# Kernel tuning notes

Hardware: AMD Instinct MI355X
Metric: run time of the kernel (lower is better)

The kernel has to match this reference:

```python
import jax, jax.numpy as jnp
import numpy as np

Nw, Nt, IN_DIM, OUT_DIM, H, FEAT = 200000, 20000, 128, 256, 8, 64
DH = OUT_DIM // H
DEG = 32
E = Nt * DEG
FFN = 512
NEG_SLOPE = 0.01  # F.leaky_relu default


def setup_inputs() -> dict:
    key = jax.random.key(0)
    ks = jax.random.split(key, 12)
    w = jax.random.normal(ks[0], (Nw, IN_DIM), jnp.float32)
    t = jax.random.normal(ks[1], (Nt, OUT_DIM), jnp.float32)
    topic_feat = jax.random.normal(ks[2], (Nt, FEAT), jnp.float32)
    edge_src = jax.random.randint(ks[3], (E,), 0, Nw)
    # every topic node gets exactly DEG in-edges (sorted dst, no empty segments)
    edge_dst = jnp.repeat(jnp.arange(Nt), DEG)
    s = lambda k, sh, f: jax.random.normal(k, sh, jnp.float32) * np.float32(f)
    fc_w = s(ks[4], (H, IN_DIM, DH), 1.0 / np.sqrt(IN_DIM))
    attn_a = s(ks[5], (H, 2 * DH), 1.0 / np.sqrt(2 * DH))
    dstfeat_w = s(ks[6], (H, FEAT, DH), 1.0 / np.sqrt(FEAT))
    proj_w = s(ks[7], (2 * OUT_DIM, OUT_DIM), 1.0 / np.sqrt(2 * OUT_DIM))
    proj_b = jnp.zeros((OUT_DIM,), jnp.float32)
    ffn_w1 = s(ks[8], (OUT_DIM, FFN), 1.0 / np.sqrt(OUT_DIM))
    ffn_b1 = jnp.zeros((FFN,), jnp.float32)
    ffn_w2 = s(ks[9], (FFN, OUT_DIM), 1.0 / np.sqrt(FFN))
    ffn_b2 = jnp.zeros((OUT_DIM,), jnp.float32)
    ln_scale = jnp.ones((OUT_DIM,), jnp.float32)
    ln_bias = jnp.zeros((OUT_DIM,), jnp.float32)
    return dict(w=w, t=t, topic_feat=topic_feat, edge_src=edge_src, edge_dst=edge_dst,
                fc_w=fc_w, attn_a=attn_a, dstfeat_w=dstfeat_w, proj_w=proj_w, proj_b=proj_b,
                ffn_w1=ffn_w1, ffn_b1=ffn_b1, ffn_w2=ffn_w2, ffn_b2=ffn_b2,
                ln_scale=ln_scale, ln_bias=ln_bias)


def reference(w, t, topic_feat, edge_src, edge_dst, fc_w, attn_a, dstfeat_w,
              proj_w, proj_b, ffn_w1, ffn_b1, ffn_w2, ffn_b2, ln_scale, ln_bias):
    # per-head projections: z on word (src) nodes, dstfeat on topic (dst) nodes
    z = jnp.einsum('ni,hid->hnd', w, fc_w)              # [H, Nw, DH]
    dz = jnp.einsum('nf,hfd->hnd', topic_feat, dstfeat_w)  # [H, Nt, DH]
    # attn_fc(cat(z_src, dstfeat)) decomposes into per-node dot products
    s_src = jnp.einsum('hnd,hd->hn', z, attn_a[:, :DH])   # [H, Nw]
    s_dst = jnp.einsum('hnd,hd->hn', dz, attn_a[:, DH:])  # [H, Nt]
    e = s_src[:, edge_src] + s_dst[:, edge_dst]           # [H, E]
    e = jnp.where(e >= 0, e, NEG_SLOPE * e)               # leaky_relu
    # segment softmax over incoming edges of each dst node (DGL mailbox softmax)
    seg_max = jax.vmap(lambda v: jax.ops.segment_max(v, edge_dst, num_segments=Nt))(e)
    seg_max = jnp.where(jnp.isfinite(seg_max), seg_max, 0.0)  # guard empty segments
    p = jnp.exp(e - seg_max[:, edge_dst])
    denom = jax.vmap(lambda v: jax.ops.segment_sum(v, edge_dst, num_segments=Nt))(p)
    alpha = p / jnp.maximum(denom[:, edge_dst], 1e-9)     # [H, E]
    msg = alpha[:, :, None] * z[:, edge_src, :]           # [H, E, DH]
    agg = jax.vmap(lambda m: jax.ops.segment_sum(m, edge_dst, num_segments=Nt))(msg)  # [H, Nt, DH]
    h = jnp.transpose(agg, (1, 0, 2)).reshape(Nt, OUT_DIM)  # head concat
    h = jax.nn.elu(h)
    h = jnp.concatenate([h, t], axis=-1) @ proj_w + proj_b  # [Nt, OUT_DIM]
    # PositionwiseFeedForward: LN -> gelu -> linear -> residual (dropout off in eval)
    mu = jnp.mean(h, axis=-1, keepdims=True)
    var = jnp.var(h, axis=-1, keepdims=True)
    xn = (h - mu) / jnp.sqrt(var + 1e-6) * ln_scale + ln_bias
    inter = jax.nn.gelu(xn @ ffn_w1 + ffn_b1, approximate=False)
    return (inter @ ffn_w2 + ffn_b2) + h
```

## Files before the change

### kernel.cpp

```cpp
#include <hip/hip_runtime.h>
#include <hip/hip_bf16.h>

typedef __attribute__((ext_vector_type(8))) short short8v;
typedef __attribute__((ext_vector_type(4))) float f32x4;

#define NW 200000
#define NT 20000
#define KIN 128
#define ODIM 256
#define NH 8
#define DH_ 32
#define FEAT_ 64
#define DEG_ 32
#define FFN_ 512

#define WS_Z     0ull
#define WS_SSRC  102400000ull
#define WS_SDST  108800000ull
#define WS_HBF   109440000ull
#define WS_TBF   119680000ull
#define WS_B1T   129920000ull
#define WS_PWT   129985536ull
#define WS_W1T   130247680ull
#define WS_W2T   130509824ull
#define WS_ABT   130771968ull

__device__ __forceinline__ unsigned short f2bf(float x) {
    __hip_bfloat16 b = __float2bfloat16(x);
    return *reinterpret_cast<unsigned short*>(&b);
}
__device__ __forceinline__ float bf2f(unsigned short u) {
    unsigned int v = ((unsigned int)u) << 16;
    return __uint_as_float(v);
}

__global__ __launch_bounds__(256) void prep_w(const float* __restrict__ fc_w,
        const float* __restrict__ proj_w, const float* __restrict__ w1,
        const float* __restrict__ w2, const float* __restrict__ attn_a,
        unsigned short* __restrict__ b1f, unsigned short* __restrict__ pwf,
        unsigned short* __restrict__ w1f, unsigned short* __restrict__ w2f,
        unsigned short* __restrict__ abt) {
    int i = blockIdx.x * 256 + threadIdx.x;
    int j = i & 7, l = (i >> 3) & 63;
    int l16 = l & 15, lq = l >> 4;
    if (i < 32768) {
        int kk = (i >> 9) & 3, g = i >> 11;
        int c = g * 16 + l16, k = kk * 32 + lq * 8 + j;
        int h = c >> 5, d = c & 31;
        b1f[i] = f2bf(fc_w[(h * KIN + k) * DH_ + d]);
    }
    if (i < 4096) {
        int h = i >> 8, k = i & 255;
        abt[i] = ((k >> 5) == h) ? f2bf(attn_a[h * 64 + (k & 31)]) : (unsigned short)0;
    }
    {
        int kk = (i >> 9) & 15, g = i >> 13;
        int c = g * 16 + l16, k = kk * 32 + lq * 8 + j;
        pwf[i] = f2bf(proj_w[(size_t)k * ODIM + c]);
    }
    {
        int kk = (i >> 9) & 7, g = i >> 12;
        int c = g * 16 + l16, k = kk * 32 + lq * 8 + j;
        w1f[i] = f2bf(w1[(size_t)k * FFN_ + c]);
    }
    {
        int kk = (i >> 9) & 15, g = i >> 13;
        int c = g * 16 + l16, k = kk * 32 + lq * 8 + j;
        w2f[i] = f2bf(w2[(size_t)k * ODIM + c]);
    }
}

__global__ __launch_bounds__(256) void prep_t(const float* __restrict__ t,
                                              unsigned short* __restrict__ tbf) {
    int i = blockIdx.x * 256 + threadIdx.x;
    const float4* p = (const float4*)(t + (size_t)i * 8);
    float4 a = p[0], b = p[1];
    short8v o;
    o[0] = (short)f2bf(a.x); o[1] = (short)f2bf(a.y);
    o[2] = (short)f2bf(a.z); o[3] = (short)f2bf(a.w);
    o[4] = (short)f2bf(b.x); o[5] = (short)f2bf(b.y);
    o[6] = (short)f2bf(b.z); o[7] = (short)f2bf(b.w);
    *((short8v*)tbf + i) = o;
}

#define ZRP 264
#define TPB 5
__global__ __launch_bounds__(256) void k1_z(const float* __restrict__ w,
        const unsigned short* __restrict__ b1f, const unsigned short* __restrict__ abt,
        unsigned short* __restrict__ z, float* __restrict__ s_src) {
    __shared__ unsigned short aS[2][64 * 136];
    __shared__ unsigned short zR[64 * ZRP];
    const int tid = threadIdx.x;
    const int wv = tid >> 6, l = tid & 63;
    const int l16 = l & 15, lq = l >> 4;
    const int tile0 = blockIdx.x * TPB;
    float4 vb[8];
    #pragma unroll
    for (int j = 0; j < 8; ++j) {
        int i = tid + j * 256;
        int r = i >> 5, kq = i & 31;
        vb[j] = *(const float4*)(w + (size_t)(tile0 * 64 + r) * KIN + kq * 4);
    }
    #pragma unroll
    for (int j = 0; j < 8; ++j) {
        int i = tid + j * 256;
        int r = i >> 5, kq = i & 31;
        ushort4 u;
        u.x = f2bf(vb[j].x); u.y = f2bf(vb[j].y);
        u.z = f2bf(vb[j].z); u.w = f2bf(vb[j].w);
        *(ushort4*)(&aS[0][r * 136 + kq * 4]) = u;
    }
    for (int t = 0; t < TPB; ++t) {
        const int cur = t & 1;
        const int row0 = (tile0 + t) * 64;
        if (t < TPB - 1) {
            #pragma unroll
            for (int j = 0; j < 8; ++j) {
                int i = tid + j * 256;
                int r = i >> 5, kq = i & 31;
                vb[j] = *(const float4*)(w + (size_t)(row0 + 64 + r) * KIN + kq * 4);
            }
        }
        __syncthreads();
        f32x4 acc[4][4];
        #pragma unroll
        for (int a = 0; a < 4; ++a)
            #pragma unroll
            for (int b = 0; b < 4; ++b)
                acc[a][b] = (f32x4){0.f, 0.f, 0.f, 0.f};
        #pragma unroll
        for (int kk = 0; kk < 4; ++kk) {
            short8v af[4], bfr[4];
            #pragma unroll
            for (int rf = 0; rf < 4; ++rf)
                af[rf] = *(const short8v*)(&aS[cur][(rf * 16 + l16) * 136 + kk * 32 + lq * 8]);
            #pragma unroll
            for (int cf = 0; cf < 4; ++cf)
                bfr[cf] = *(const short8v*)((const short*)b1f +
                            ((((wv * 4 + cf) * 4 + kk) << 9) + l * 8));
            #pragma unroll
            for (int rf = 0; rf < 4; ++rf)
                #pragma unroll
                for (int cf = 0; cf < 4; ++cf)
                    acc[rf][cf] = __builtin_amdgcn_mfma_f32_16x16x32_bf16(
                        af[rf], bfr[cf], acc[rf][cf], 0, 0, 0);
        }
        #pragma unroll
        for (int rl = 0; rl < 4; ++rl)
            #pragma unroll
            for (int cf = 0; cf < 4; ++cf) {
                int c = wv * 64 + cf * 16 + l16;
                #pragma unroll
                for (int q = 0; q < 4; ++q) {
                    int row = rl * 16 + lq * 4 + q;
                    int pc = c ^ ((row & 8) << 1);
                    zR[row * ZRP + pc] = f2bf(acc[rl][cf][q]);
                }
            }
        __syncthreads();
        {
            const int base = wv * 16;
            const int rsw = (l16 & 8) << 1;
            f32x4 sacc = (f32x4){0.f, 0.f, 0.f, 0.f};
            #pragma unroll
            for (int kk = 0; kk < 8; ++kk) {
                int kc = (kk * 32 + lq * 8) ^ rsw;
                short8v a = *(const short8v*)(&zR[(base + l16) * ZRP + kc]);
                short8v b = *(const short8v*)((const short*)abt + (size_t)l16 * 256 + kk * 32 + lq * 8);
                sacc = __builtin_amdgcn_mfma_f32_16x16x32_bf16(a, b, sacc, 0, 0, 0);
            }
            if (l16 < NH) {
                #pragma unroll
                for (int q = 0; q < 4; ++q)
                    s_src[(size_t)(row0 + base + lq * 4 + q) * NH + l16] = sacc[q];
            }
        }
        #pragma unroll
        for (int j = 0; j < 8; ++j) {
            int idx = tid + j * 256;
            int r = idx >> 5, ch = idx & 31;
            int pc = (ch * 8) ^ ((r & 8) << 1);
            short8v v = *(const short8v*)(&zR[r * ZRP + pc]);
            *(short8v*)(z + (size_t)(row0 + r) * ODIM + ch * 8) = v;
        }
        if (t < TPB - 1) {
            #pragma unroll
            for (int j = 0; j < 8; ++j) {
                int i = tid + j * 256;
                int r = i >> 5, kq = i & 31;
                ushort4 u;
                u.x = f2bf(vb[j].x); u.y = f2bf(vb[j].y);
                u.z = f2bf(vb[j].z); u.w = f2bf(vb[j].w);
                *(ushort4*)(&aS[cur ^ 1][r * 136 + kq * 4]) = u;
            }
        }
    }
}

__global__ __launch_bounds__(256) void k_sdst(const float* __restrict__ topic_feat,
        const float* __restrict__ dstfeat_w, const float* __restrict__ attn_a,
        float* __restrict__ s_dst) {
    __shared__ float rS[NH * 65];
    __shared__ float tfS[32 * 65];
    const int tid = threadIdx.x;
    for (int i = tid; i < NH * FEAT_; i += 256) {
        int h = i >> 6, f = i & 63;
        const float* dw = dstfeat_w + (size_t)(h * FEAT_ + f) * DH_;
        const float* aa = attn_a + h * 64 + DH_;
        float s = 0.f;
        #pragma unroll
        for (int d = 0; d < DH_; ++d) s += dw[d] * aa[d];
        rS[h * 65 + f] = s;
    }
    const int n0 = blockIdx.x * 32;
    for (int i = tid; i < 32 * FEAT_; i += 256) {
        int n = i >> 6, f = i & 63;
        tfS[n * 65 + f] = topic_feat[(size_t)(n0 + n) * FEAT_ + f];
    }
    __syncthreads();
    int n = tid >> 3, h = tid & 7;
    float s = 0.f;
    #pragma unroll
    for (int f = 0; f < FEAT_; ++f) s += tfS[n * 65 + f] * rS[h * 65 + f];
    s_dst[(size_t)(n0 + n) * NH + h] = s;
}

__global__ __launch_bounds__(256) void k2_attn(const int* __restrict__ edge_src,
        const float* __restrict__ s_src, const float* __restrict__ s_dst,
        const unsigned short* __restrict__ z, unsigned short* __restrict__ hbf) {
    __shared__ int srcS[4][32];
    __shared__ float aS[4][32][8];
    const int tid = threadIdx.x;
    const int nd = tid >> 6, l = tid & 63;
    const int n = blockIdx.x * 4 + nd;
    if (l < 32) srcS[nd][l] = edge_src[(size_t)n * DEG_ + l];
    __syncthreads();
    {
        int e = l & 31, h0 = (l >> 5) * 4;
        int s = srcS[nd][e];
        float4 ss = *(const float4*)(s_src + (size_t)s * NH + h0);
        float4 sd = *(const float4*)(s_dst + (size_t)n * NH + h0);
        float v[4] = {ss.x + sd.x, ss.y + sd.y, ss.z + sd.z, ss.w + sd.w};
        #pragma unroll
        for (int j = 0; j < 4; ++j) v[j] = (v[j] >= 0.f) ? v[j] : 0.01f * v[j];
        float al[4];
        #pragma unroll
        for (int j = 0; j < 4; ++j) {
            float m = v[j];
            #pragma unroll
            for (int off = 16; off >= 1; off >>= 1)
                m = fmaxf(m, __shfl_xor(m, off));
            float p = expf(v[j] - m);
            float su = p;
            #pragma unroll
            for (int off = 16; off >= 1; off >>= 1)
                su += __shfl_xor(su, off);
            al[j] = p / fmaxf(su, 1e-9f);
        }
        float4 a4 = {al[0], al[1], al[2], al[3]};
        *(float4*)(&aS[nd][e][h0]) = a4;
    }
    __syncthreads();
    {
        const int half = l >> 5, cl = l & 31;
        const int head = cl >> 2;
        float acc[8];
        #pragma unroll
        for (int j = 0; j < 8; ++j) acc[j] = 0.f;
        #pragma unroll 4
        for (int ee = 0; ee < 16; ++ee) {
            int e = ee * 2 + half;
            float a = aS[nd][e][head];
            int sp = srcS[nd][e];
            short8v zv = *(const short8v*)(z + (size_t)sp * ODIM + cl * 8);
            #pragma unroll
            for (int j = 0; j < 8; ++j)
                acc[j] += a * bf2f((unsigned short)zv[j]);
        }
        #pragma unroll
        for (int j = 0; j < 8; ++j)
            acc[j] += __shfl_xor(acc[j], 32);
        if (half == 0) {
            short8v o;
            #pragma unroll
            for (int j = 0; j < 8; ++j) {
                float v = (acc[j] > 0.f) ? acc[j] : expm1f(acc[j]);
                o[j] = (short)f2bf(v);
            }
            *(short8v*)(hbf + (size_t)n * ODIM + cl * 8) = o;
        }
    }
}

#define BUFP 524
#define XNP  268
__global__ __launch_bounds__(256, 3) void k34_ffn(const unsigned short* __restrict__ hbf,
        const unsigned short* __restrict__ tbf, const unsigned short* __restrict__ pwf,
        const float* __restrict__ proj_b, const float* __restrict__ ln_scale,
        const float* __restrict__ ln_bias, const unsigned short* __restrict__ w1f,
        const float* __restrict__ b1, const unsigned short* __restrict__ w2f,
        const float* __restrict__ b2, float* __restrict__ out) {
    __shared__ unsigned short buf[32 * BUFP];
    __shared__ unsigned short xnS[32 * XNP];
    __shared__ float lnP[4][32], lnQ[4][32];
    __shared__ float muS[32], rsS[32];
    const int tid = threadIdx.x;
    const int row0 = blockIdx.x * 32;
    #pragma unroll
    for (int j = 0; j < 8; ++j) {
        int i = tid + j * 256;
        int r = i >> 6, cq = i & 63;
        ushort4 hv = *(const ushort4*)(hbf + (size_t)(row0 + r) * ODIM + cq * 4);
        *(ushort4*)(&buf[r * BUFP + cq * 4]) = hv;
        ushort4 tv = *(const ushort4*)(tbf + (size_t)(row0 + r) * ODIM + cq * 4);
        *(ushort4*)(&buf[r * BUFP + 256 + cq * 4]) = tv;
    }
    __syncthreads();
    const int wv = tid >> 6, l = tid & 63;
    const int l16 = l & 15, lq = l >> 4;
    const int l8 = l * 8;
    f32x4 acc0[2][4];
    #pragma unroll
    for (int rf = 0; rf < 2; ++rf)
        #pragma unroll
        for (int cf = 0; cf < 4; ++cf) acc0[rf][cf] = (f32x4){0.f, 0.f, 0.f, 0.f};
    {
        short8v bp[2][4];
        #pragma unroll
        for (int cf = 0; cf < 4; ++cf)
            bp[0][cf] = *(const short8v*)((const short*)pwf + ((((wv * 4 + cf) * 16) << 9) + l8));
        #pragma unroll
        for (int kk = 0; kk < 16; ++kk) {
            const int cur = kk & 1;
            if (kk < 15) {
                #pragma unroll
                for (int cf = 0; cf < 4; ++cf)
                    bp[cur ^ 1][cf] = *(const short8v*)((const short*)pwf +
                        ((((wv * 4 + cf) * 16 + kk + 1) << 9) + l8));
            }
            short8v a0 = *(const short8v*)(&buf[l16 * BUFP + kk * 32 + lq * 8]);
            short8v a1 = *(const short8v*)(&buf[(16 + l16) * BUFP + kk * 32 + lq * 8]);
            #pragma unroll
            for (int cf = 0; cf < 4; ++cf) {
                acc0[0][cf] = __builtin_amdgcn_mfma_f32_16x16x32_bf16(a0, bp[cur][cf], acc0[0][cf], 0, 0, 0);
                acc0[1][cf] = __builtin_amdgcn_mfma_f32_16x16x32_bf16(a1, bp[cur][cf], acc0[1][cf], 0, 0, 0);
            }
        }
    }
    #pragma unroll
    for (int cf = 0; cf < 4; ++cf) {
        float bb = proj_b[wv * 64 + cf * 16 + l16];
        #pragma unroll
        for (int rf = 0; rf < 2; ++rf)
            #pragma unroll
            for (int q = 0; q < 4; ++q) acc0[rf][cf][q] += bb;
    }
    #pragma unroll
    for (int rf = 0; rf < 2; ++rf)
        #pragma unroll
        for (int q = 0; q < 4; ++q) {
            float s = 0.f, s2 = 0.f;
            #pragma unroll
            for (int cf = 0; cf < 4; ++cf) {
                float v = acc0[rf][cf][q];
                s += v; s2 += v * v;
            }
            s  += __shfl_xor(s, 1);  s2 += __shfl_xor(s2, 1);
            s  += __shfl_xor(s, 2);  s2 += __shfl_xor(s2, 2);
            s  += __shfl_xor(s, 4);  s2 += __shfl_xor(s2, 4);
            s  += __shfl_xor(s, 8);  s2 += __shfl_xor(s2, 8);
            if (l16 == 0) {
                int row = rf * 16 + lq * 4 + q;
                lnP[wv][row] = s; lnQ[wv][row] = s2;
            }
        }
    __syncthreads();
    if (tid < 32) {
        float s = lnP[0][tid] + lnP[1][tid] + lnP[2][tid] + lnP[3][tid];
        float s2 = lnQ[0][tid] + lnQ[1][tid] + lnQ[2][tid] + lnQ[3][tid];
        float mu = s * (1.f / 256.f);
        float var = s2 * (1.f / 256.f) - mu * mu;
        muS[tid] = mu;
        rsS[tid] = rsqrtf(var + 1e-6f);
    }
    __syncthreads();
    #pragma unroll
    for (int cf = 0; cf < 4; ++cf) {
        int c = wv * 64 + cf * 16 + l16;
        float ls = ln_scale[c], lb = ln_bias[c];
        #pragma unroll
        for (int rf = 0; rf < 2; ++rf)
            #pragma unroll
            for (int q = 0; q < 4; ++q) {
                int row = rf * 16 + lq * 4 + q;
                float x = (acc0[rf][cf][q] - muS[row]) * rsS[row] * ls + lb;
                xnS[row * XNP + c] = f2bf(x);
            }
    }
    __syncthreads();
    {
        f32x4 acc1[2][8];
        #pragma unroll
        for (int rf = 0; rf < 2; ++rf)
            #pragma unroll
            for (int cf = 0; cf < 8; ++cf) acc1[rf][cf] = (f32x4){0.f, 0.f, 0.f, 0.f};
        #pragma unroll 2
        for (int kk = 0; kk < 8; ++kk) {
            short8v a0 = *(const short8v*)(&xnS[l16 * XNP + kk * 32 + lq * 8]);
            short8v a1 = *(const short8v*)(&xnS[(16 + l16) * XNP + kk * 32 + lq * 8]);
            #pragma unroll
            for (int cf = 0; cf < 8; ++cf) {
                short8v b = *(const short8v*)((const short*)w1f +
                    ((((wv * 8 + cf) * 8 + kk) << 9) + l8));
                acc1[0][cf] = __builtin_amdgcn_mfma_f32_16x16x32_bf16(a0, b, acc1[0][cf], 0, 0, 0);
                acc1[1][cf] = __builtin_amdgcn_mfma_f32_16x16x32_bf16(a1, b, acc1[1][cf], 0, 0, 0);
            }
        }
        #pragma unroll
        for (int cf = 0; cf < 8; ++cf) {
            int c = wv * 128 + cf * 16 + l16;
            float bb = b1[c];
            #pragma unroll
            for (int rf = 0; rf < 2; ++rf)
                #pragma unroll
                for (int q = 0; q < 4; ++q) {
                    float x = acc1[rf][cf][q] + bb;
                    x = 0.5f * x * (1.f + erff(x * 0.70710678118654752f));
                    buf[(rf * 16 + lq * 4 + q) * BUFP + c] = f2bf(x);
                }
        }
    }
    __syncthreads();
    {
        f32x4 acc2[2][4];
        #pragma unroll
        for (int rf = 0; rf < 2; ++rf)
            #pragma unroll
            for (int cf = 0; cf < 4; ++cf) acc2[rf][cf] = (f32x4){0.f, 0.f, 0.f, 0.f};
        short8v bp[2][4];
        #pragma unroll
        for (int cf = 0; cf < 4; ++cf)
            bp[0][cf] = *(const short8v*)((const short*)w2f + ((((wv * 4 + cf) * 16) << 9) + l8));
        #pragma unroll
        for (int kk = 0; kk < 16; ++kk) {
            const int cur = kk & 1;
            if (kk < 15) {
                #pragma unroll
                for (int cf = 0; cf < 4; ++cf)
                    bp[cur ^ 1][cf] = *(const short8v*)((const short*)w2f +
                        ((((wv * 4 + cf) * 16 + kk + 1) << 9) + l8));
            }
            short8v a0 = *(const short8v*)(&buf[l16 * BUFP + kk * 32 + lq * 8]);
            short8v a1 = *(const short8v*)(&buf[(16 + l16) * BUFP + kk * 32 + lq * 8]);
            #pragma unroll
            for (int cf = 0; cf < 4; ++cf) {
                acc2[0][cf] = __builtin_amdgcn_mfma_f32_16x16x32_bf16(a0, bp[cur][cf], acc2[0][cf], 0, 0, 0);
                acc2[1][cf] = __builtin_amdgcn_mfma_f32_16x16x32_bf16(a1, bp[cur][cf], acc2[1][cf], 0, 0, 0);
            }
        }
        #pragma unroll
        for (int cf = 0; cf < 4; ++cf) {
            int c = wv * 64 + cf * 16 + l16;
            float bb = b2[c];
            #pragma unroll
            for (int rf = 0; rf < 2; ++rf)
                #pragma unroll
                for (int q = 0; q < 4; ++q) {
                    int row = rf * 16 + lq * 4 + q;
                    out[(size_t)(row0 + row) * ODIM + c] =
                        acc2[rf][cf][q] + bb + acc0[rf][cf][q];
                }
        }
    }
}

extern "C" void kernel_launch(void* const* d_in, const int* in_sizes, int n_in,
                              void* d_out, int out_size, void* d_ws, size_t ws_size,
                              hipStream_t stream) {
    const float* w          = (const float*)d_in[0];
    const float* t          = (const float*)d_in[1];
    const float* topic_feat = (const float*)d_in[2];
    const int*   edge_src   = (const int*)d_in[3];
    const float* fc_w       = (const float*)d_in[5];
    const float* attn_a     = (const float*)d_in[6];
    const float* dstfeat_w  = (const float*)d_in[7];
    const float* proj_w     = (const float*)d_in[8];
    const float* proj_b     = (const float*)d_in[9];
    const float* ffn_w1     = (const float*)d_in[10];
    const float* ffn_b1     = (const float*)d_in[11];
    const float* ffn_w2     = (const float*)d_in[12];
    const float* ffn_b2     = (const float*)d_in[13];
    const float* ln_scale   = (const float*)d_in[14];
    const float* ln_bias    = (const float*)d_in[15];
    float* out = (float*)d_out;

    char* ws = (char*)d_ws;
    unsigned short* z    = (unsigned short*)(ws + WS_Z);
    float* s_src         = (float*)(ws + WS_SSRC);
    float* s_dst         = (float*)(ws + WS_SDST);
    unsigned short* hbf  = (unsigned short*)(ws + WS_HBF);
    unsigned short* tbf  = (unsigned short*)(ws + WS_TBF);
    unsigned short* b1f  = (unsigned short*)(ws + WS_B1T);
    unsigned short* pwf  = (unsigned short*)(ws + WS_PWT);
    unsigned short* w1f  = (unsigned short*)(ws + WS_W1T);
    unsigned short* w2f  = (unsigned short*)(ws + WS_W2T);
    unsigned short* abt  = (unsigned short*)(ws + WS_ABT);

    hipLaunchKernelGGL(prep_w, dim3(512),           dim3(256), 0, stream,
                       fc_w, proj_w, ffn_w1, ffn_w2, attn_a, b1f, pwf, w1f, w2f, abt);
    hipLaunchKernelGGL(prep_t, dim3(2500),          dim3(256), 0, stream, t, tbf);
    hipLaunchKernelGGL(k1_z,   dim3(NW / (64*TPB)), dim3(256), 0, stream,
                       w, b1f, abt, z, s_src);
    hipLaunchKernelGGL(k_sdst, dim3(NT / 32),       dim3(256), 0, stream,
                       topic_feat, dstfeat_w, attn_a, s_dst);
    hipLaunchKernelGGL(k2_attn, dim3(NT / 4),       dim3(256), 0, stream,
                       edge_src, s_src, s_dst, z, hbf);
    hipLaunchKernelGGL(k34_ffn, dim3(NT / 32),      dim3(256), 0, stream,
                       hbf, tbf, pwf, proj_b, ln_scale, ln_bias,
                       w1f, ffn_b1, w2f, ffn_b2, out);
}
```

Measured before the change: 187.6 us.

## Store z in MFMA-native permuted layout and compute s_src from accumulators

The z projection kernel no longer stages results through a shared-memory tile. It writes bf16 z straight from MFMA accumulators in a permuted per-tile layout, and s_src is now a shuffle-reduced dot product in registers instead of a second MFMA pass. The attention gather uses the new layout to find z rows, and proj_w rows are permuted in prep so the channel order of the head concat still matches. This removes the LDS round trip and two barriers per tile, and TPB drops to 3 with a tail guard. The risk is that each gathered row is now spread across scattered 16-byte chunks, which may hurt gather coalescing, and the index bookkeeping is fragile.

```diff
diff --git a/kernel.cpp b/kernel.cpp
--- a/kernel.cpp
+++ b/kernel.cpp
@@ -13,6 +13,7 @@
 #define FEAT_ 64
 #define DEG_ 32
 #define FFN_ 512
+#define NTILE 3125
 
 #define WS_Z     0ull
 #define WS_SSRC  102400000ull
@@ -23,7 +24,6 @@
 #define WS_PWT   129985536ull
 #define WS_W1T   130247680ull
 #define WS_W2T   130509824ull
-#define WS_ABT   130771968ull
 
 __device__ __forceinline__ unsigned short f2bf(float x) {
     __hip_bfloat16 b = __float2bfloat16(x);
@@ -36,10 +36,9 @@
 
 __global__ __launch_bounds__(256) void prep_w(const float* __restrict__ fc_w,
         const float* __restrict__ proj_w, const float* __restrict__ w1,
-        const float* __restrict__ w2, const float* __restrict__ attn_a,
+        const float* __restrict__ w2,
         unsigned short* __restrict__ b1f, unsigned short* __restrict__ pwf,
-        unsigned short* __restrict__ w1f, unsigned short* __restrict__ w2f,
-        unsigned short* __restrict__ abt) {
+        unsigned short* __restrict__ w1f, unsigned short* __restrict__ w2f) {
     int i = blockIdx.x * 256 + threadIdx.x;
     int j = i & 7, l = (i >> 3) & 63;
     int l16 = l & 15, lq = l >> 4;
@@ -49,14 +48,13 @@
         int h = c >> 5, d = c & 31;
         b1f[i] = f2bf(fc_w[(h * KIN + k) * DH_ + d]);
     }
-    if (i < 4096) {
-        int h = i >> 8, k = i & 255;
-        abt[i] = ((k >> 5) == h) ? f2bf(attn_a[h * 64 + (k & 31)]) : (unsigned short)0;
-    }
     {
         int kk = (i >> 9) & 15, g = i >> 13;
         int c = g * 16 + l16, k = kk * 32 + lq * 8 + j;
-        pwf[i] = f2bf(proj_w[(size_t)k * ODIM + c]);
+        int kp = k;
+        if (k < 256)
+            kp = ((k >> 6) << 6) + (k & 3) * 16 + 2 * ((k >> 3) & 7) + ((k >> 2) & 1);
+        pwf[i] = f2bf(proj_w[(size_t)kp * ODIM + c]);
     }
     {
         int kk = (i >> 9) & 7, g = i >> 12;
@@ -83,17 +81,16 @@
     *((short8v*)tbf + i) = o;
 }
 
-#define ZRP 264
-#define TPB 5
+#define TPB 3
 __global__ __launch_bounds__(256) void k1_z(const float* __restrict__ w,
-        const unsigned short* __restrict__ b1f, const unsigned short* __restrict__ abt,
+        const unsigned short* __restrict__ b1f, const float* __restrict__ attn_a,
         unsigned short* __restrict__ z, float* __restrict__ s_src) {
     __shared__ unsigned short aS[2][64 * 136];
-    __shared__ unsigned short zR[64 * ZRP];
     const int tid = threadIdx.x;
     const int wv = tid >> 6, l = tid & 63;
     const int l16 = l & 15, lq = l >> 4;
     const int tile0 = blockIdx.x * TPB;
+    const int ntile = min(TPB, NTILE - tile0);
     float4 vb[8];
     #pragma unroll
     for (int j = 0; j < 8; ++j) {
@@ -110,10 +107,15 @@
         u.z = f2bf(vb[j].z); u.w = f2bf(vb[j].w);
         *(ushort4*)(&aS[0][r * 136 + kq * 4]) = u;
     }
-    for (int t = 0; t < TPB; ++t) {
+    const float ca0 = attn_a[(wv * 2 + 0) * 64 + l16];
+    const float cb0 = attn_a[(wv * 2 + 0) * 64 + 16 + l16];
+    const float ca1 = attn_a[(wv * 2 + 1) * 64 + l16];
+    const float cb1 = attn_a[(wv * 2 + 1) * 64 + 16 + l16];
+    for (int t = 0; t < ntile; ++t) {
         const int cur = t & 1;
-        const int row0 = (tile0 + t) * 64;
-        if (t < TPB - 1) {
+        const int tile = tile0 + t;
+        const int row0 = tile * 64;
+        if (t < ntile - 1) {
             #pragma unroll
             for (int j = 0; j < 8; ++j) {
                 int i = tid + j * 256;
@@ -146,44 +148,33 @@
                         af[rf], bfr[cf], acc[rf][cf], 0, 0, 0);
         }
         #pragma unroll
+        for (int rf = 0; rf < 4; ++rf)
+            #pragma unroll
+            for (int q = 0; q < 4; ++q) {
+                float s0 = acc[rf][0][q] * ca0 + acc[rf][1][q] * cb0;
+                float s1 = acc[rf][2][q] * ca1 + acc[rf][3][q] * cb1;
+                s0 += __shfl_xor(s0, 1); s1 += __shfl_xor(s1, 1);
+                s0 += __shfl_xor(s0, 2); s1 += __shfl_xor(s1, 2);
+                s0 += __shfl_xor(s0, 4); s1 += __shfl_xor(s1, 4);
+                s0 += __shfl_xor(s0, 8); s1 += __shfl_xor(s1, 8);
+                if (l16 == 0) {
+                    size_t row = (size_t)row0 + rf * 16 + lq * 4 + q;
+                    s_src[row * NH + wv * 2]     = s0;
+                    s_src[row * NH + wv * 2 + 1] = s1;
+                }
+            }
+        #pragma unroll
         for (int rl = 0; rl < 4; ++rl)
             #pragma unroll
-            for (int cf = 0; cf < 4; ++cf) {
-                int c = wv * 64 + cf * 16 + l16;
-                #pragma unroll
-                for (int q = 0; q < 4; ++q) {
-                    int row = rl * 16 + lq * 4 + q;
-                    int pc = c ^ ((row & 8) << 1);
-                    zR[row * ZRP + pc] = f2bf(acc[rl][cf][q]);
-                }
-            }
-        __syncthreads();
-        {
-            const int base = wv * 16;
-            const int rsw = (l16 & 8) << 1;
-            f32x4 sacc = (f32x4){0.f, 0.f, 0.f, 0.f};
-            #pragma unroll
-            for (int kk = 0; kk < 8; ++kk) {
-                int kc = (kk * 32 + lq * 8) ^ rsw;
-                short8v a = *(const short8v*)(&zR[(base + l16) * ZRP + kc]);
-                short8v b = *(const short8v*)((const short*)abt + (size_t)l16 * 256 + kk * 32 + lq * 8);
-                sacc = __builtin_amdgcn_mfma_f32_16x16x32_bf16(a, b, sacc, 0, 0, 0);
-            }
-            if (l16 < NH) {
-                #pragma unroll
-                for (int q = 0; q < 4; ++q)
-                    s_src[(size_t)(row0 + base + lq * 4 + q) * NH + l16] = sacc[q];
-            }
-        }
-        #pragma unroll
-        for (int j = 0; j < 8; ++j) {
-            int idx = tid + j * 256;
-            int r = idx >> 5, ch = idx & 31;
-            int pc = (ch * 8) ^ ((r & 8) << 1);
-            short8v v = *(const short8v*)(&zR[r * ZRP + pc]);
-            *(short8v*)(z + (size_t)(row0 + r) * ODIM + ch * 8) = v;
-        }
-        if (t < TPB - 1) {
+            for (int q = 0; q < 4; ++q) {
+                ushort4 u;
+                u.x = f2bf(acc[rl][0][q]); u.y = f2bf(acc[rl][1][q]);
+                u.z = f2bf(acc[rl][2][q]); u.w = f2bf(acc[rl][3][q]);
+                size_t a4 = (size_t)tile * 4096 +
+                            (size_t)((((wv * 4 + rl) * 4 + q) * 4 + lq) * 16 + l16);
+                ((ushort4*)z)[a4] = u;
+            }
+        if (t < ntile - 1) {
             #pragma unroll
             for (int j = 0; j < 8; ++j) {
                 int i = tid + j * 256;
@@ -263,19 +254,25 @@
     __syncthreads();
     {
         const int half = l >> 5, cl = l & 31;
-        const int head = cl >> 2;
+        const int wvh = cl >> 3, h0 = wvh * 2;
+        const int lo8 = (cl & 7) * 8;
         float acc[8];
         #pragma unroll
         for (int j = 0; j < 8; ++j) acc[j] = 0.f;
         #pragma unroll 4
         for (int ee = 0; ee < 16; ++ee) {
             int e = ee * 2 + half;
-            float a = aS[nd][e][head];
             int sp = srcS[nd][e];
-            short8v zv = *(const short8v*)(z + (size_t)sp * ODIM + cl * 8);
-            #pragma unroll
-            for (int j = 0; j < 8; ++j)
-                acc[j] += a * bf2f((unsigned short)zv[j]);
+            float a_lo = aS[nd][e][h0], a_hi = aS[nd][e][h0 + 1];
+            int rr = sp & 63;
+            size_t off = (size_t)(sp >> 6) * 16384 +
+                (size_t)(((((wvh * 4 + (rr >> 4)) * 4 + (rr & 3)) * 4 + ((rr >> 2) & 3)) * 64) + lo8);
+            short8v zv = *(const short8v*)(z + off);
+            #pragma unroll
+            for (int u = 0; u < 8; ++u) {
+                float a = ((u >> 1) & 1) ? a_hi : a_lo;
+                acc[u] += a * bf2f((unsigned short)zv[u]);
+            }
         }
         #pragma unroll
         for (int j = 0; j < 8; ++j)
@@ -504,18 +501,17 @@
     unsigned short* pwf  = (unsigned short*)(ws + WS_PWT);
     unsigned short* w1f  = (unsigned short*)(ws + WS_W1T);
     unsigned short* w2f  = (unsigned short*)(ws + WS_W2T);
-    unsigned short* abt  = (unsigned short*)(ws + WS_ABT);
-
-    hipLaunchKernelGGL(prep_w, dim3(512),           dim3(256), 0, stream,
-                       fc_w, proj_w, ffn_w1, ffn_w2, attn_a, b1f, pwf, w1f, w2f, abt);
-    hipLaunchKernelGGL(prep_t, dim3(2500),          dim3(256), 0, stream, t, tbf);
-    hipLaunchKernelGGL(k1_z,   dim3(NW / (64*TPB)), dim3(256), 0, stream,
-                       w, b1f, abt, z, s_src);
-    hipLaunchKernelGGL(k_sdst, dim3(NT / 32),       dim3(256), 0, stream,
+
+    hipLaunchKernelGGL(prep_w, dim3(512),  dim3(256), 0, stream,
+                       fc_w, proj_w, ffn_w1, ffn_w2, b1f, pwf, w1f, w2f);
+    hipLaunchKernelGGL(prep_t, dim3(2500), dim3(256), 0, stream, t, tbf);
+    hipLaunchKernelGGL(k1_z,   dim3((NTILE + TPB - 1) / TPB), dim3(256), 0, stream,
+                       w, b1f, attn_a, z, s_src);
+    hipLaunchKernelGGL(k_sdst, dim3(NT / 32), dim3(256), 0, stream,
                        topic_feat, dstfeat_w, attn_a, s_dst);
-    hipLaunchKernelGGL(k2_attn, dim3(NT / 4),       dim3(256), 0, stream,
+    hipLaunchKernelGGL(k2_attn, dim3(NT / 4), dim3(256), 0, stream,
                        edge_src, s_src, s_dst, z, hbf);
-    hipLaunchKernelGGL(k34_ffn, dim3(NT / 32),      dim3(256), 0, stream,
+    hipLaunchKernelGGL(k34_ffn, dim3(NT / 32), dim3(256), 0, stream,
                        hbf, tbf, pwf, proj_b, ln_scale, ln_bias,
                        w1f, ffn_b1, w2f, ffn_b2, out);
 }
```

After: 221.9 us. 1.18x slower.

## Permute z column layout to vectorize LDS stores and drop XOR swizzle

Applied to the files above, without the earlier changes.

Stores z in a permuted column order so each lane writes its four accumulator columns as one ushort4 LDS store instead of sixteen scalar swizzled stores. The attention-score weight matrix and the projection weight rows are permuted to match the new layout. In the gather kernel, each lane's 8 contiguous stored columns now span two heads, so it selects between two attention weights. Removing the XOR swizzle may bring back LDS bank conflicts on the reads.

```diff
diff --git a/kernel.cpp b/kernel.cpp
--- a/kernel.cpp
+++ b/kernel.cpp
@@ -24,6 +24,7 @@
 #define WS_W1T   130247680ull
 #define WS_W2T   130509824ull
 #define WS_ABT   130771968ull
+
 
 __device__ __forceinline__ unsigned short f2bf(float x) {
     __hip_bfloat16 b = __float2bfloat16(x);
@@ -50,13 +51,17 @@
         b1f[i] = f2bf(fc_w[(h * KIN + k) * DH_ + d]);
     }
     if (i < 4096) {
-        int h = i >> 8, k = i & 255;
-        abt[i] = ((k >> 5) == h) ? f2bf(attn_a[h * 64 + (k & 31)]) : (unsigned short)0;
+        int h = i >> 8, p = i & 255;
+        int c = (p >> 6) * 64 + (p & 3) * 16 + ((p >> 2) & 15);
+        abt[i] = ((c >> 5) == h) ? f2bf(attn_a[h * 64 + (c & 31)]) : (unsigned short)0;
     }
     {
         int kk = (i >> 9) & 15, g = i >> 13;
         int c = g * 16 + l16, k = kk * 32 + lq * 8 + j;
-        pwf[i] = f2bf(proj_w[(size_t)k * ODIM + c]);
+        int kp = k;
+        if (k < 256)
+            kp = ((k >> 6) << 6) + (k & 3) * 16 + ((k >> 2) & 15);
+        pwf[i] = f2bf(proj_w[(size_t)kp * ODIM + c]);
     }
     {
         int kk = (i >> 9) & 7, g = i >> 12;
@@ -148,24 +153,20 @@
         #pragma unroll
         for (int rl = 0; rl < 4; ++rl)
             #pragma unroll
-            for (int cf = 0; cf < 4; ++cf) {
-                int c = wv * 64 + cf * 16 + l16;
-                #pragma unroll
-                for (int q = 0; q < 4; ++q) {
-                    int row = rl * 16 + lq * 4 + q;
-                    int pc = c ^ ((row & 8) << 1);
-                    zR[row * ZRP + pc] = f2bf(acc[rl][cf][q]);
-                }
+            for (int q = 0; q < 4; ++q) {
+                int row = rl * 16 + lq * 4 + q;
+                ushort4 u;
+                u.x = f2bf(acc[rl][0][q]); u.y = f2bf(acc[rl][1][q]);
+                u.z = f2bf(acc[rl][2][q]); u.w = f2bf(acc[rl][3][q]);
+                *(ushort4*)(&zR[row * ZRP + wv * 64 + l16 * 4]) = u;
             }
         __syncthreads();
         {
             const int base = wv * 16;
-            const int rsw = (l16 & 8) << 1;
             f32x4 sacc = (f32x4){0.f, 0.f, 0.f, 0.f};
             #pragma unroll
             for (int kk = 0; kk < 8; ++kk) {
-                int kc = (kk * 32 + lq * 8) ^ rsw;
-                short8v a = *(const short8v*)(&zR[(base + l16) * ZRP + kc]);
+                short8v a = *(const short8v*)(&zR[(base + l16) * ZRP + kk * 32 + lq * 8]);
                 short8v b = *(const short8v*)((const short*)abt + (size_t)l16 * 256 + kk * 32 + lq * 8);
                 sacc = __builtin_amdgcn_mfma_f32_16x16x32_bf16(a, b, sacc, 0, 0, 0);
             }
@@ -179,8 +180,7 @@
         for (int j = 0; j < 8; ++j) {
             int idx = tid + j * 256;
             int r = idx >> 5, ch = idx & 31;
-            int pc = (ch * 8) ^ ((r & 8) << 1);
-            short8v v = *(const short8v*)(&zR[r * ZRP + pc]);
+            short8v v = *(const short8v*)(&zR[r * ZRP + ch * 8]);
             *(short8v*)(z + (size_t)(row0 + r) * ODIM + ch * 8) = v;
         }
         if (t < TPB - 1) {
@@ -263,19 +263,21 @@
     __syncthreads();
     {
         const int half = l >> 5, cl = l & 31;
-        const int head = cl >> 2;
+        const int h0 = (cl >> 3) * 2;
         float acc[8];
         #pragma unroll
         for (int j = 0; j < 8; ++j) acc[j] = 0.f;
         #pragma unroll 4
         for (int ee = 0; ee < 16; ++ee) {
             int e = ee * 2 + half;
-            float a = aS[nd][e][head];
             int sp = srcS[nd][e];
+            float a_lo = aS[nd][e][h0], a_hi = aS[nd][e][h0 + 1];
             short8v zv = *(const short8v*)(z + (size_t)sp * ODIM + cl * 8);
             #pragma unroll
-            for (int j = 0; j < 8; ++j)
-                acc[j] += a * bf2f((unsigned short)zv[j]);
+            for (int u = 0; u < 8; ++u) {
+                float a = ((u >> 1) & 1) ? a_hi : a_lo;
+                acc[u] += a * bf2f((unsigned short)zv[u]);
+            }
         }
         #pragma unroll
         for (int j = 0; j < 8; ++j)
```

New measurement: 181.5 us. 3.3% less time.
